# Kernel optimization log

Measured on AMD Instinct MI355X. Metric: run time of the kernel, lower is better.

## Reference

```python
import jax, jax.numpy as jnp
import numpy as np

D_IN = 4096
NUM_HEADS = 32
NUM_KV_GROUPS = 8
HEAD_DIM = D_IN // NUM_HEADS  # 128 (init overwrites head_dim)
GROUP_SIZE = NUM_HEADS // NUM_KV_GROUPS
SEQ = 2048
BATCH = 1
EPS = 1e-6


def layernorm(t, w, b):
    mu = jnp.mean(t, axis=-1, keepdims=True)
    var = jnp.var(t, axis=-1, keepdims=True)
    return (t - mu) * jax.lax.rsqrt(var + EPS) * w + b


def rope(t, cos, sin):
    # t: [B, H, S, D]; cos/sin: [S, D] broadcast over B, H
    half = t.shape[-1] // 2
    x1, x2 = t[..., :half], t[..., half:]
    rot = jnp.concatenate([-x2, x1], axis=-1)
    return t * cos + rot * sin


def setup_inputs() -> dict:
    key = jax.random.key(0)
    ks = jax.random.split(key, 10)
    x = jax.random.normal(ks[0], (BATCH, SEQ, D_IN), dtype=jnp.float32)
    mask = jnp.triu(jnp.ones((SEQ, SEQ), dtype=bool), k=1)  # True = masked (causal)
    # RoPE tables
    inv_freq = 1.0 / (10000.0 ** (np.arange(0, HEAD_DIM, 2, dtype=np.float32) / HEAD_DIM))
    pos = np.arange(SEQ, dtype=np.float32)
    ang = np.einsum('s,d->sd', pos, inv_freq)  # [S, D/2]
    ang = np.concatenate([ang, ang], axis=-1)  # [S, D]
    cos = jnp.asarray(np.cos(ang))
    sin = jnp.asarray(np.sin(ang))
    s = 0.02
    Wq = jax.random.normal(ks[1], (D_IN, NUM_HEADS * HEAD_DIM), dtype=jnp.float32) * s
    Wk = jax.random.normal(ks[2], (D_IN, NUM_KV_GROUPS * HEAD_DIM), dtype=jnp.float32) * s
    Wv = jax.random.normal(ks[3], (D_IN, NUM_KV_GROUPS * HEAD_DIM), dtype=jnp.float32) * s
    Wo = jax.random.normal(ks[4], (NUM_HEADS * HEAD_DIM, D_IN), dtype=jnp.float32) * s
    qn_w = jnp.ones((HEAD_DIM,), jnp.float32)
    qn_b = jnp.zeros((HEAD_DIM,), jnp.float32)
    kn_w = jnp.ones((HEAD_DIM,), jnp.float32)
    kn_b = jnp.zeros((HEAD_DIM,), jnp.float32)
    return {"x": x, "mask": mask, "cos": cos, "sin": sin, "Wq": Wq, "Wk": Wk,
            "Wv": Wv, "Wo": Wo, "qn_w": qn_w, "qn_b": qn_b, "kn_w": kn_w, "kn_b": kn_b}


def reference(x, mask, cos, sin, Wq, Wk, Wv, Wo, qn_w, qn_b, kn_w, kn_b):
    B, S, _ = x.shape
    q = (x @ Wq).reshape(B, S, NUM_HEADS, HEAD_DIM).transpose(0, 2, 1, 3)      # [B,H,S,D]
    k = (x @ Wk).reshape(B, S, NUM_KV_GROUPS, HEAD_DIM).transpose(0, 2, 1, 3)  # [B,G,S,D]
    v = (x @ Wv).reshape(B, S, NUM_KV_GROUPS, HEAD_DIM).transpose(0, 2, 1, 3)
    q = layernorm(q, qn_w, qn_b)
    k = layernorm(k, kn_w, kn_b)
    q = rope(q, cos, sin)
    k = rope(k, cos, sin)
    k = jnp.repeat(k, GROUP_SIZE, axis=1)  # [B,H,S,D]
    v = jnp.repeat(v, GROUP_SIZE, axis=1)
    scores = jnp.einsum('bhqd,bhkd->bhqk', q, k)
    scores = jnp.where(mask, -jnp.inf, scores)
    attn = jax.nn.softmax(scores / jnp.sqrt(jnp.float32(HEAD_DIM)), axis=-1)
    ctx = jnp.einsum('bhqk,bhkd->bhqd', attn, v)
    ctx = ctx.transpose(0, 2, 1, 3).reshape(B, S, NUM_HEADS * HEAD_DIM)
    return ctx @ Wo
```

## Files before the change

### kernel.cpp

```cpp
#include <hip/hip_runtime.h>
#include <stdint.h>

#define SQ   2048
#define DIN  4096
#define NH   32
#define NKV  8
#define HD   128
#define NQKV 6144

typedef float f32x4 __attribute__((ext_vector_type(4)));
typedef short bf16x8 __attribute__((ext_vector_type(8)));

__device__ __forceinline__ short f2bf(float f) {
  union { float f; uint32_t u; } v; v.f = f;
  uint32_t r = (v.u + 0x7FFFu + ((v.u >> 16) & 1u)) >> 16;
  return (short)r;
}

__device__ __forceinline__ void gl2lds(const void* g, void* l) {
  __builtin_amdgcn_global_load_lds(
      (const __attribute__((address_space(1))) void*)g,
      (__attribute__((address_space(3))) void*)l, 16, 0, 0);
}

__global__ void cvt_bf16(const float* __restrict__ src, short* __restrict__ dst, long n) {
  long i = ((long)blockIdx.x * blockDim.x + threadIdx.x) * 4;
  if (i + 3 < n) {
    float4 v = *(const float4*)(src + i);
    short o[4] = { f2bf(v.x), f2bf(v.y), f2bf(v.z), f2bf(v.w) };
    *(uint2*)(dst + i) = *(uint2*)o;
  }
}

__global__ __launch_bounds__(256) void transpose_cvt(const float* __restrict__ src, int ldS, long zS,
                                                     short* __restrict__ dst, int ldD, long zD) {
  __shared__ float tile[64][65];
  src += (long)blockIdx.z * zS;
  dst += (long)blockIdx.z * zD;
  int r0 = blockIdx.y * 64, c0 = blockIdx.x * 64;
  int tid = threadIdx.x;
#pragma unroll
  for (int i = 0; i < 16; ++i) {
    int idx = i * 256 + tid;
    int rr = idx >> 6, cc = idx & 63;
    tile[rr][cc] = src[(long)(r0 + rr) * ldS + c0 + cc];
  }
  __syncthreads();
#pragma unroll
  for (int i = 0; i < 16; ++i) {
    int idx = i * 256 + tid;
    int dr = idx >> 6, dc = idx & 63;
    dst[(long)(c0 + dr) * ldD + r0 + dc] = f2bf(tile[dc][dr]);
  }
}

#define TSZ 24576
#define MFMA(d, a, b) d = __builtin_amdgcn_mfma_f32_16x16x32_bf16(a, b, d, 0, 0, 0)

__global__ __launch_bounds__(512, 2) void gemm8p(const short* __restrict__ A, const short* __restrict__ Bt,
                                                 float* __restrict__ C, int M, int N, int K) {
  __shared__ __align__(16) short lds[3 * TSZ];
  int nwg = gridDim.x;
  int lin = ((int)blockIdx.x & 7) * (nwg >> 3) + ((int)blockIdx.x >> 3);
  int mt = M >> 7;
  int m0 = (lin % mt) * 128, n0 = (lin / mt) * 256;

  int tid = threadIdx.x;
  int w = tid >> 6, lane = tid & 63;
  int l16 = lane & 15, lq = lane >> 4;
  int wm = (w >> 2) * 64, wn = (w & 3) * 64;
  int sx = l16 & 7;
  int fo0 = ((lq ^ sx) << 3) + (l16 << 6);
  int fo1 = (((lq + 4) ^ sx) << 3) + (l16 << 6);

  int srow = lane >> 3;
  int g8 = (lane & 7) ^ srow;
  long a8K = 8L * K;
  const short* aS = A + (long)(m0 + w * 16 + srow) * K + g8 * 8;
  const short* bS = Bt + (long)(n0 + w * 32 + srow) * K + g8 * 8;

  f32x4 acc[4][4] = {};
  const int KT = K >> 6;

#pragma unroll
  for (int tt = 0; tt < 2; ++tt) {
    short* base = lds + tt * TSZ;
    gl2lds(aS + tt * 64, base + (w * 2) * 512);
    gl2lds(aS + a8K + tt * 64, base + (w * 2 + 1) * 512);
#pragma unroll
    for (int j = 0; j < 4; ++j)
      gl2lds(bS + j * a8K + tt * 64, base + 8192 + (w * 4 + j) * 512);
  }
  asm volatile("s_waitcnt vmcnt(6)" ::: "memory");
  __builtin_amdgcn_s_barrier();

  for (int t = 0; t < KT; ++t) {
    const short* wA = lds + (t % 3) * TSZ + wm * 64;
    const short* wB = lds + (t % 3) * TSZ + 8192 + wn * 64;
    int sb = (t + 2) % 3;
    short* stA = lds + sb * TSZ + (w * 2) * 512;
    short* stB = lds + sb * TSZ + 8192 + (w * 4) * 512;
    long ko = (long)(t + 2) * 64;
    bool doStage = (t + 2 < KT);

    bf16x8 aAk0, aAk1, aBk0, aBk1, bAk0, bAk1, bBk0, bBk1;

    aAk0 = *(const bf16x8*)(wA + fo0);        aAk1 = *(const bf16x8*)(wA + fo1);
    aBk0 = *(const bf16x8*)(wA + 1024 + fo0); aBk1 = *(const bf16x8*)(wA + 1024 + fo1);
    bAk0 = *(const bf16x8*)(wB + fo0);        bAk1 = *(const bf16x8*)(wB + fo1);
    bBk0 = *(const bf16x8*)(wB + 1024 + fo0); bBk1 = *(const bf16x8*)(wB + 1024 + fo1);
    if (doStage) { gl2lds(bS + ko, stB); gl2lds(bS + a8K + ko, stB + 512); }
    __builtin_amdgcn_s_barrier();
    asm volatile("s_waitcnt lgkmcnt(0)" ::: "memory");
    __builtin_amdgcn_s_setprio(1);
    MFMA(acc[0][0], aAk0, bAk0); MFMA(acc[0][1], aAk0, bBk0);
    MFMA(acc[1][0], aBk0, bAk0); MFMA(acc[1][1], aBk0, bBk0);
    MFMA(acc[0][0], aAk1, bAk1); MFMA(acc[0][1], aAk1, bBk1);
    MFMA(acc[1][0], aBk1, bAk1); MFMA(acc[1][1], aBk1, bBk1);
    __builtin_amdgcn_s_setprio(0);
    __builtin_amdgcn_s_barrier();

    bAk0 = *(const bf16x8*)(wB + 2048 + fo0); bAk1 = *(const bf16x8*)(wB + 2048 + fo1);
    bBk0 = *(const bf16x8*)(wB + 3072 + fo0); bBk1 = *(const bf16x8*)(wB + 3072 + fo1);
    if (doStage) { gl2lds(bS + 2 * a8K + ko, stB + 1024); gl2lds(bS + 3 * a8K + ko, stB + 1536); }
    __builtin_amdgcn_s_barrier();
    asm volatile("s_waitcnt lgkmcnt(0)" ::: "memory");
    __builtin_amdgcn_s_setprio(1);
    MFMA(acc[0][2], aAk0, bAk0); MFMA(acc[0][3], aAk0, bBk0);
    MFMA(acc[1][2], aBk0, bAk0); MFMA(acc[1][3], aBk0, bBk0);
    MFMA(acc[0][2], aAk1, bAk1); MFMA(acc[0][3], aAk1, bBk1);
    MFMA(acc[1][2], aBk1, bAk1); MFMA(acc[1][3], aBk1, bBk1);
    __builtin_amdgcn_s_setprio(0);
    __builtin_amdgcn_s_barrier();

    aAk0 = *(const bf16x8*)(wA + 2048 + fo0); aAk1 = *(const bf16x8*)(wA + 2048 + fo1);
    aBk0 = *(const bf16x8*)(wA + 3072 + fo0); aBk1 = *(const bf16x8*)(wA + 3072 + fo1);
    if (doStage) { gl2lds(aS + ko, stA); }
    __builtin_amdgcn_s_barrier();
    asm volatile("s_waitcnt lgkmcnt(0)" ::: "memory");
    __builtin_amdgcn_s_setprio(1);
    MFMA(acc[2][2], aAk0, bAk0); MFMA(acc[2][3], aAk0, bBk0);
    MFMA(acc[3][2], aBk0, bAk0); MFMA(acc[3][3], aBk0, bBk0);
    MFMA(acc[2][2], aAk1, bAk1); MFMA(acc[2][3], aAk1, bBk1);
    MFMA(acc[3][2], aBk1, bAk1); MFMA(acc[3][3], aBk1, bBk1);
    __builtin_amdgcn_s_setprio(0);
    __builtin_amdgcn_s_barrier();

    bAk0 = *(const bf16x8*)(wB + fo0);        bAk1 = *(const bf16x8*)(wB + fo1);
    bBk0 = *(const bf16x8*)(wB + 1024 + fo0); bBk1 = *(const bf16x8*)(wB + 1024 + fo1);
    if (doStage) { gl2lds(aS + a8K + ko, stA + 512); }
    __builtin_amdgcn_s_barrier();
    asm volatile("s_waitcnt lgkmcnt(0)" ::: "memory");
    __builtin_amdgcn_s_setprio(1);
    MFMA(acc[2][0], aAk0, bAk0); MFMA(acc[2][1], aAk0, bBk0);
    MFMA(acc[3][0], aBk0, bAk0); MFMA(acc[3][1], aBk0, bBk0);
    MFMA(acc[2][0], aAk1, bAk1); MFMA(acc[2][1], aAk1, bBk1);
    MFMA(acc[3][0], aBk1, bAk1); MFMA(acc[3][1], aBk1, bBk1);
    __builtin_amdgcn_s_setprio(0);
    if (t < KT - 1) {
      if (doStage) asm volatile("s_waitcnt vmcnt(6)" ::: "memory");
      else         asm volatile("s_waitcnt vmcnt(0)" ::: "memory");
      __builtin_amdgcn_s_barrier();
    }
  }

#pragma unroll
  for (int i = 0; i < 4; ++i)
#pragma unroll
    for (int j = 0; j < 4; ++j)
#pragma unroll
      for (int r = 0; r < 4; ++r)
        C[(long)(m0 + wm + i * 16 + lq * 4 + r) * N + n0 + wn + j * 16 + l16] = acc[i][j][r];
}

__global__ __launch_bounds__(64) void ln_rope(const float* __restrict__ qkv,
                                              const float* __restrict__ cosb, const float* __restrict__ sinb,
                                              const float* __restrict__ qw, const float* __restrict__ qb,
                                              const float* __restrict__ kw, const float* __restrict__ kb,
                                              short* __restrict__ qo, short* __restrict__ ko) {
  int s = blockIdx.x, slice = blockIdx.y, t = threadIdx.x;
  bool isq = slice < NH;
  int off = isq ? slice * HD : DIN + (slice - NH) * HD;
  const float* src = qkv + (long)s * NQKV + off;
  float v0 = src[t], v1 = src[t + 64];
  float sum = v0 + v1, ss = v0 * v0 + v1 * v1;
#pragma unroll
  for (int o = 1; o < 64; o <<= 1) { sum += __shfl_xor(sum, o); ss += __shfl_xor(ss, o); }
  float mu = sum * (1.f / 128.f);
  float var = ss * (1.f / 128.f) - mu * mu;
  float rstd = rsqrtf(var + 1e-6f);
  const float* w  = isq ? qw : kw;
  const float* bb = isq ? qb : kb;
  float n0 = (v0 - mu) * rstd * w[t]      + bb[t];
  float n1 = (v1 - mu) * rstd * w[t + 64] + bb[t + 64];
  float c0 = cosb[s * HD + t], c1 = cosb[s * HD + t + 64];
  float s0 = sinb[s * HD + t], s1 = sinb[s * HD + t + 64];
  float o0 = n0 * c0 - n1 * s0;
  float o1 = n1 * c1 + n0 * s1;
  short* dst = isq ? (qo + ((long)slice * SQ + s) * HD)
                   : (ko + ((long)(slice - NH) * SQ + s) * HD);
  dst[t] = f2bf(o0);
  dst[t + 64] = f2bf(o1);
}

__global__ __launch_bounds__(256) void attn(const short* __restrict__ q, const short* __restrict__ k,
                                            const short* __restrict__ vT, short* __restrict__ ctx) {
  int pair = blockIdx.x, h = blockIdx.y, g = h >> 2;
  int tid = threadIdx.x, w = tid >> 6, lane = tid & 63;
  int l16 = lane & 15, lq = lane >> 4;
  __shared__ __align__(16) short Ks[64 * 128];
  __shared__ __align__(16) short Vs[128 * 64];
  __shared__ __align__(16) short pbuf[4][16 * 72];
  const short* qh = q + (long)h * SQ * HD;
  const short* kg = k + (long)g * SQ * HD;
  const short* vg = vT + (long)g * HD * SQ;
  int kr = (w * 4) * 4 + (lane >> 4);
  int vrw = (w * 4) * 8 + (lane >> 3);
  const float sc = 0.08838834764831845f * 1.4426950408889634f;

  for (int st = 0; st < 2; ++st) {
    int qt = st ? (31 - pair) : pair;
    int qbase = qt * 64 + w * 16;
    bf16x8 aq[4];
#pragma unroll
    for (int kk = 0; kk < 4; ++kk)
      aq[kk] = *(const bf16x8*)&qh[(long)(qbase + l16) * HD + kk * 32 + lq * 8];
    float m_r[4], l_r[4];
    f32x4 acc[8] = {};
#pragma unroll
    for (int r = 0; r < 4; ++r) { m_r[r] = -__builtin_inff(); l_r[r] = 0.f; }

    for (int kt = 0; kt <= qt; ++kt) {
#pragma unroll
      for (int j = 0; j < 4; ++j) {
        int call = w * 4 + j;
        int r = kr + j * 4;
        int chk = (lane & 15) ^ (r & 15);
        gl2lds(&kg[(long)(kt * 64 + r) * HD + chk * 8], &Ks[call * 512]);
        int rv = vrw + j * 8;
        int chv = (lane & 7) ^ (rv & 7);
        gl2lds(&vg[(long)rv * SQ + kt * 64 + chv * 8], &Vs[call * 512]);
      }
      __syncthreads();
      f32x4 s4[4];
#pragma unroll
      for (int b = 0; b < 4; ++b) s4[b] = (f32x4){0.f, 0.f, 0.f, 0.f};
#pragma unroll
      for (int b = 0; b < 4; ++b) {
        int krow = b * 16 + l16;
#pragma unroll
        for (int kk = 0; kk < 4; ++kk) {
          bf16x8 bk = *(const bf16x8*)&Ks[krow * 128 + ((kk * 4 + lq) ^ (krow & 15)) * 8];
          s4[b] = __builtin_amdgcn_mfma_f32_16x16x32_bf16(aq[kk], bk, s4[b], 0, 0, 0);
        }
      }
      int qrow0 = qbase + lq * 4;
#pragma unroll
      for (int b = 0; b < 4; ++b) {
        int key = kt * 64 + b * 16 + l16;
#pragma unroll
        for (int r = 0; r < 4; ++r) {
          float val = s4[b][r] * sc;
          s4[b][r] = (key > qrow0 + r) ? -__builtin_inff() : val;
        }
      }
      float p[4][4];
#pragma unroll
      for (int r = 0; r < 4; ++r) {
        float mx = fmaxf(fmaxf(s4[0][r], s4[1][r]), fmaxf(s4[2][r], s4[3][r]));
#pragma unroll
        for (int o = 1; o < 16; o <<= 1) mx = fmaxf(mx, __shfl_xor(mx, o));
        float mnew = fmaxf(m_r[r], mx);
        float alpha = exp2f(m_r[r] - mnew);
        float sum = 0.f;
#pragma unroll
        for (int b = 0; b < 4; ++b) { float pv = exp2f(s4[b][r] - mnew); p[b][r] = pv; sum += pv; }
#pragma unroll
        for (int o = 1; o < 16; o <<= 1) sum += __shfl_xor(sum, o);
        l_r[r] = l_r[r] * alpha + sum;
        m_r[r] = mnew;
#pragma unroll
        for (int n = 0; n < 8; ++n) acc[n][r] *= alpha;
      }
#pragma unroll
      for (int b = 0; b < 4; ++b)
#pragma unroll
        for (int r = 0; r < 4; ++r)
          pbuf[w][(lq * 4 + r) * 72 + b * 16 + l16] = f2bf(p[b][r]);
#pragma unroll
      for (int kk = 0; kk < 2; ++kk) {
        bf16x8 pf = *(const bf16x8*)&pbuf[w][l16 * 72 + kk * 32 + lq * 8];
#pragma unroll
        for (int n = 0; n < 8; ++n) {
          int vrow = n * 16 + l16;
          bf16x8 vf = *(const bf16x8*)&Vs[vrow * 64 + ((kk * 4 + lq) ^ (vrow & 7)) * 8];
          acc[n] = __builtin_amdgcn_mfma_f32_16x16x32_bf16(pf, vf, acc[n], 0, 0, 0);
        }
      }
      __syncthreads();
    }
#pragma unroll
    for (int n = 0; n < 8; ++n)
#pragma unroll
      for (int r = 0; r < 4; ++r) {
        int srow = qbase + lq * 4 + r;
        ctx[(long)srow * (NH * HD) + h * HD + n * 16 + l16] = f2bf(acc[n][r] / l_r[r]);
      }
  }
}

#define XB_OFF     0L
#define QR_OFF     0L
#define WQKVT_OFF  16777216L
#define KR_OFF     16777216L
#define VT_OFF     20971520L
#define CTX_OFF    25165824L
#define WOT_OFF    67108864L
#define QKV_OFF    100663296L

extern "C" void kernel_launch(void* const* d_in, const int* in_sizes, int n_in,
                              void* d_out, int out_size, void* d_ws, size_t ws_size,
                              hipStream_t stream) {
  const float* x    = (const float*)d_in[0];
  const float* cosb = (const float*)d_in[2];
  const float* sinb = (const float*)d_in[3];
  const float* Wq   = (const float*)d_in[4];
  const float* Wk   = (const float*)d_in[5];
  const float* Wv   = (const float*)d_in[6];
  const float* Wo   = (const float*)d_in[7];
  const float* qnw  = (const float*)d_in[8];
  const float* qnb  = (const float*)d_in[9];
  const float* knw  = (const float*)d_in[10];
  const float* knb  = (const float*)d_in[11];

  char* ws = (char*)d_ws;
  short* xb    = (short*)(ws + XB_OFF);
  short* qr    = (short*)(ws + QR_OFF);
  short* wqkvt = (short*)(ws + WQKVT_OFF);
  short* krp   = (short*)(ws + KR_OFF);
  short* vt    = (short*)(ws + VT_OFF);
  short* ctx   = (short*)(ws + CTX_OFF);
  short* wot   = (short*)(ws + WOT_OFF);
  float* qkv   = (float*)(ws + QKV_OFF);

  cvt_bf16<<<8192, 256, 0, stream>>>(x, xb, (long)SQ * DIN);
  transpose_cvt<<<dim3(64, 64, 1), 256, 0, stream>>>(Wq, 4096, 0L, wqkvt, 4096, 0L);
  transpose_cvt<<<dim3(16, 64, 1), 256, 0, stream>>>(Wk, 1024, 0L, wqkvt + (long)4096 * 4096, 4096, 0L);
  transpose_cvt<<<dim3(16, 64, 1), 256, 0, stream>>>(Wv, 1024, 0L, wqkvt + (long)5120 * 4096, 4096, 0L);
  transpose_cvt<<<dim3(64, 64, 1), 256, 0, stream>>>(Wo, 4096, 0L, wot, 4096, 0L);
  gemm8p<<<(SQ / 128) * (NQKV / 256), 512, 0, stream>>>(xb, wqkvt, qkv, SQ, NQKV, DIN);
  ln_rope<<<dim3(SQ, NH + NKV), 64, 0, stream>>>(qkv, cosb, sinb, qnw, qnb, knw, knb, qr, krp);
  transpose_cvt<<<dim3(2, 32, 8), 256, 0, stream>>>(qkv + 5120, NQKV, 128L, vt, SQ, (long)HD * SQ);
  attn<<<dim3(16, NH), 256, 0, stream>>>(qr, krp, vt, ctx);
  gemm8p<<<(SQ / 128) * (DIN / 256), 512, 0, stream>>>(ctx, wot, (float*)d_out, SQ, DIN, DIN);
}
```

Baseline: 584.1 us.

## Enlarge GEMM tile to 256x256 with double-buffered half-K LDS staging

The bf16 GEMM used for the QKV and output projections now computes a 256x256 output tile per workgroup instead of 128x256. Each wave holds 8x4 accumulator fragments. The LDS pipeline moves from a triple buffer of full 64-wide K tiles to a double buffer where each K step is split into two 32-wide halves that are staged separately, with a new swizzle. The aim is more operand reuse per LDS load and less global traffic per FLOP. In exchange it needs more accumulator registers, and with half as many workgroups per GEMM the GPU's compute units are filled less evenly.

```diff
diff --git a/kernel.cpp b/kernel.cpp
--- a/kernel.cpp
+++ b/kernel.cpp
@@ -54,118 +54,110 @@
   }
 }
 
-#define TSZ 24576
+#define HBUF  8192
+#define BUFSZ 32768
 #define MFMA(d, a, b) d = __builtin_amdgcn_mfma_f32_16x16x32_bf16(a, b, d, 0, 0, 0)
+
+#define SA(t, h) { short* d = &lds[(((t) & 1) * BUFSZ) + (h) * HBUF + dA]; \
+                   const short* s = aS + (long)(t) * 64 + (h) * 32;        \
+                   gl2lds(s, d); gl2lds(s + K16, d + 512); }
+#define SB(t, h) { short* d = &lds[(((t) & 1) * BUFSZ) + (h) * HBUF + dB]; \
+                   const short* s = bS + (long)(t) * 64 + (h) * 32;        \
+                   gl2lds(s, d); gl2lds(s + K16, d + 512); }
 
 __global__ __launch_bounds__(512, 2) void gemm8p(const short* __restrict__ A, const short* __restrict__ Bt,
                                                  float* __restrict__ C, int M, int N, int K) {
-  __shared__ __align__(16) short lds[3 * TSZ];
+  __shared__ __align__(16) short lds[2 * BUFSZ];
   int nwg = gridDim.x;
   int lin = ((int)blockIdx.x & 7) * (nwg >> 3) + ((int)blockIdx.x >> 3);
-  int mt = M >> 7;
-  int m0 = (lin % mt) * 128, n0 = (lin / mt) * 256;
+  int mt = M >> 8;
+  int m0 = (lin % mt) << 8, n0 = (lin / mt) << 8;
 
   int tid = threadIdx.x;
   int w = tid >> 6, lane = tid & 63;
   int l16 = lane & 15, lq = lane >> 4;
-  int wm = (w >> 2) * 64, wn = (w & 3) * 64;
-  int sx = l16 & 7;
-  int fo0 = ((lq ^ sx) << 3) + (l16 << 6);
-  int fo1 = (((lq + 4) ^ sx) << 3) + (l16 << 6);
-
-  int srow = lane >> 3;
-  int g8 = (lane & 7) ^ srow;
-  long a8K = 8L * K;
-  const short* aS = A + (long)(m0 + w * 16 + srow) * K + g8 * 8;
-  const short* bS = Bt + (long)(n0 + w * 32 + srow) * K + g8 * 8;
-
-  f32x4 acc[4][4] = {};
+  int wm = (w >> 2) << 7;
+  int wn = (w & 3) << 6;
+
+  int fl = (l16 & 3) ^ ((l16 >> 2) & 1);
+  int aoff = (wm + l16) * 32 + ((lq ^ fl) << 3);
+  int boff = 2 * HBUF + (wn + l16) * 32 + ((lq ^ fl) << 3);
+
+  int grow = lane >> 2;
+  int gch = (lane & 3) ^ ((grow & 3) ^ ((grow >> 2) & 1));
+  const short* aS = A + (long)(m0 + 32 * w + grow) * K + gch * 8;
+  const short* bS = Bt + (long)(n0 + 32 * w + grow) * K + gch * 8;
+  long K16 = 16L * K;
+  int dA = 1024 * w;
+  int dB = 2 * HBUF + 1024 * w;
+
+  f32x4 acc[8][4] = {};
   const int KT = K >> 6;
 
-#pragma unroll
-  for (int tt = 0; tt < 2; ++tt) {
-    short* base = lds + tt * TSZ;
-    gl2lds(aS + tt * 64, base + (w * 2) * 512);
-    gl2lds(aS + a8K + tt * 64, base + (w * 2 + 1) * 512);
-#pragma unroll
-    for (int j = 0; j < 4; ++j)
-      gl2lds(bS + j * a8K + tt * 64, base + 8192 + (w * 4 + j) * 512);
-  }
-  asm volatile("s_waitcnt vmcnt(6)" ::: "memory");
+  SA(0, 0); SB(0, 0); SA(0, 1); SB(0, 1); SA(1, 0); SB(1, 0);
+  asm volatile("s_waitcnt vmcnt(4)" ::: "memory");
   __builtin_amdgcn_s_barrier();
 
   for (int t = 0; t < KT; ++t) {
-    const short* wA = lds + (t % 3) * TSZ + wm * 64;
-    const short* wB = lds + (t % 3) * TSZ + 8192 + wn * 64;
-    int sb = (t + 2) % 3;
-    short* stA = lds + sb * TSZ + (w * 2) * 512;
-    short* stB = lds + sb * TSZ + 8192 + (w * 4) * 512;
-    long ko = (long)(t + 2) * 64;
-    bool doStage = (t + 2 < KT);
-
-    bf16x8 aAk0, aAk1, aBk0, aBk1, bAk0, bAk1, bBk0, bBk1;
-
-    aAk0 = *(const bf16x8*)(wA + fo0);        aAk1 = *(const bf16x8*)(wA + fo1);
-    aBk0 = *(const bf16x8*)(wA + 1024 + fo0); aBk1 = *(const bf16x8*)(wA + 1024 + fo1);
-    bAk0 = *(const bf16x8*)(wB + fo0);        bAk1 = *(const bf16x8*)(wB + fo1);
-    bBk0 = *(const bf16x8*)(wB + 1024 + fo0); bBk1 = *(const bf16x8*)(wB + 1024 + fo1);
-    if (doStage) { gl2lds(bS + ko, stB); gl2lds(bS + a8K + ko, stB + 512); }
+    const short* buf = &lds[(t & 1) * BUFSZ];
+    bool s1 = (t + 1 < KT), s2 = (t + 2 < KT);
+    bf16x8 af[8], bfr[4];
+
+#pragma unroll
+    for (int i = 0; i < 8; ++i) af[i] = *(const bf16x8*)&buf[aoff + i * 512];
+    bfr[0] = *(const bf16x8*)&buf[boff];
+    bfr[1] = *(const bf16x8*)&buf[boff + 512];
+    if (s1) SA(t + 1, 1);
     __builtin_amdgcn_s_barrier();
     asm volatile("s_waitcnt lgkmcnt(0)" ::: "memory");
     __builtin_amdgcn_s_setprio(1);
-    MFMA(acc[0][0], aAk0, bAk0); MFMA(acc[0][1], aAk0, bBk0);
-    MFMA(acc[1][0], aBk0, bAk0); MFMA(acc[1][1], aBk0, bBk0);
-    MFMA(acc[0][0], aAk1, bAk1); MFMA(acc[0][1], aAk1, bBk1);
-    MFMA(acc[1][0], aBk1, bAk1); MFMA(acc[1][1], aBk1, bBk1);
+#pragma unroll
+    for (int i = 0; i < 8; ++i) { MFMA(acc[i][0], af[i], bfr[0]); MFMA(acc[i][1], af[i], bfr[1]); }
     __builtin_amdgcn_s_setprio(0);
     __builtin_amdgcn_s_barrier();
 
-    bAk0 = *(const bf16x8*)(wB + 2048 + fo0); bAk1 = *(const bf16x8*)(wB + 2048 + fo1);
-    bBk0 = *(const bf16x8*)(wB + 3072 + fo0); bBk1 = *(const bf16x8*)(wB + 3072 + fo1);
-    if (doStage) { gl2lds(bS + 2 * a8K + ko, stB + 1024); gl2lds(bS + 3 * a8K + ko, stB + 1536); }
+    bfr[2] = *(const bf16x8*)&buf[boff + 1024];
+    bfr[3] = *(const bf16x8*)&buf[boff + 1536];
+    if (s1) SB(t + 1, 1);
     __builtin_amdgcn_s_barrier();
     asm volatile("s_waitcnt lgkmcnt(0)" ::: "memory");
     __builtin_amdgcn_s_setprio(1);
-    MFMA(acc[0][2], aAk0, bAk0); MFMA(acc[0][3], aAk0, bBk0);
-    MFMA(acc[1][2], aBk0, bAk0); MFMA(acc[1][3], aBk0, bBk0);
-    MFMA(acc[0][2], aAk1, bAk1); MFMA(acc[0][3], aAk1, bBk1);
-    MFMA(acc[1][2], aBk1, bAk1); MFMA(acc[1][3], aBk1, bBk1);
+#pragma unroll
+    for (int i = 0; i < 8; ++i) { MFMA(acc[i][2], af[i], bfr[2]); MFMA(acc[i][3], af[i], bfr[3]); }
     __builtin_amdgcn_s_setprio(0);
     __builtin_amdgcn_s_barrier();
 
-    aAk0 = *(const bf16x8*)(wA + 2048 + fo0); aAk1 = *(const bf16x8*)(wA + 2048 + fo1);
-    aBk0 = *(const bf16x8*)(wA + 3072 + fo0); aBk1 = *(const bf16x8*)(wA + 3072 + fo1);
-    if (doStage) { gl2lds(aS + ko, stA); }
+#pragma unroll
+    for (int i = 0; i < 8; ++i) af[i] = *(const bf16x8*)&buf[HBUF + aoff + i * 512];
+    bfr[2] = *(const bf16x8*)&buf[HBUF + boff + 1024];
+    bfr[3] = *(const bf16x8*)&buf[HBUF + boff + 1536];
+    if (s2) SA(t + 2, 0);
     __builtin_amdgcn_s_barrier();
     asm volatile("s_waitcnt lgkmcnt(0)" ::: "memory");
     __builtin_amdgcn_s_setprio(1);
-    MFMA(acc[2][2], aAk0, bAk0); MFMA(acc[2][3], aAk0, bBk0);
-    MFMA(acc[3][2], aBk0, bAk0); MFMA(acc[3][3], aBk0, bBk0);
-    MFMA(acc[2][2], aAk1, bAk1); MFMA(acc[2][3], aAk1, bBk1);
-    MFMA(acc[3][2], aBk1, bAk1); MFMA(acc[3][3], aBk1, bBk1);
+#pragma unroll
+    for (int i = 0; i < 8; ++i) { MFMA(acc[i][2], af[i], bfr[2]); MFMA(acc[i][3], af[i], bfr[3]); }
     __builtin_amdgcn_s_setprio(0);
     __builtin_amdgcn_s_barrier();
 
-    bAk0 = *(const bf16x8*)(wB + fo0);        bAk1 = *(const bf16x8*)(wB + fo1);
-    bBk0 = *(const bf16x8*)(wB + 1024 + fo0); bBk1 = *(const bf16x8*)(wB + 1024 + fo1);
-    if (doStage) { gl2lds(aS + a8K + ko, stA + 512); }
+    bfr[0] = *(const bf16x8*)&buf[HBUF + boff];
+    bfr[1] = *(const bf16x8*)&buf[HBUF + boff + 512];
+    if (s2) SB(t + 2, 0);
     __builtin_amdgcn_s_barrier();
     asm volatile("s_waitcnt lgkmcnt(0)" ::: "memory");
     __builtin_amdgcn_s_setprio(1);
-    MFMA(acc[2][0], aAk0, bAk0); MFMA(acc[2][1], aAk0, bBk0);
-    MFMA(acc[3][0], aBk0, bAk0); MFMA(acc[3][1], aBk0, bBk0);
-    MFMA(acc[2][0], aAk1, bAk1); MFMA(acc[2][1], aAk1, bBk1);
-    MFMA(acc[3][0], aBk1, bAk1); MFMA(acc[3][1], aBk1, bBk1);
+#pragma unroll
+    for (int i = 0; i < 8; ++i) { MFMA(acc[i][0], af[i], bfr[0]); MFMA(acc[i][1], af[i], bfr[1]); }
     __builtin_amdgcn_s_setprio(0);
     if (t < KT - 1) {
-      if (doStage) asm volatile("s_waitcnt vmcnt(6)" ::: "memory");
-      else         asm volatile("s_waitcnt vmcnt(0)" ::: "memory");
+      if (t == KT - 2) asm volatile("s_waitcnt vmcnt(0)" ::: "memory");
+      else             asm volatile("s_waitcnt vmcnt(4)" ::: "memory");
       __builtin_amdgcn_s_barrier();
     }
   }
 
 #pragma unroll
-  for (int i = 0; i < 4; ++i)
+  for (int i = 0; i < 8; ++i)
 #pragma unroll
     for (int j = 0; j < 4; ++j)
 #pragma unroll
@@ -348,9 +340,9 @@
   transpose_cvt<<<dim3(16, 64, 1), 256, 0, stream>>>(Wk, 1024, 0L, wqkvt + (long)4096 * 4096, 4096, 0L);
   transpose_cvt<<<dim3(16, 64, 1), 256, 0, stream>>>(Wv, 1024, 0L, wqkvt + (long)5120 * 4096, 4096, 0L);
   transpose_cvt<<<dim3(64, 64, 1), 256, 0, stream>>>(Wo, 4096, 0L, wot, 4096, 0L);
-  gemm8p<<<(SQ / 128) * (NQKV / 256), 512, 0, stream>>>(xb, wqkvt, qkv, SQ, NQKV, DIN);
+  gemm8p<<<(SQ / 256) * (NQKV / 256), 512, 0, stream>>>(xb, wqkvt, qkv, SQ, NQKV, DIN);
   ln_rope<<<dim3(SQ, NH + NKV), 64, 0, stream>>>(qkv, cosb, sinb, qnw, qnb, knw, knb, qr, krp);
   transpose_cvt<<<dim3(2, 32, 8), 256, 0, stream>>>(qkv + 5120, NQKV, 128L, vt, SQ, (long)HD * SQ);
   attn<<<dim3(16, NH), 256, 0, stream>>>(qr, krp, vt, ctx);
-  gemm8p<<<(SQ / 128) * (DIN / 256), 512, 0, stream>>>(ctx, wot, (float*)d_out, SQ, DIN, DIN);
-}
+  gemm8p<<<(SQ / 256) * (DIN / 256), 512, 0, stream>>>(ctx, wot, (float*)d_out, SQ, DIN, DIN);
+}
```

Measured after the change: 616.0 us. 1.05x slower.
